# Performance work log

Measured on AMD Instinct MI355X. Metric: run time of the kernel, lower is better.

Reference implementation:

```python
import jax, jax.numpy as jnp
import numpy as np

B, S, D, H = 4, 2048, 1024, 16
DK = D // H
THETA = 10000.0


def apply_rope(x, pos, theta):
    # x: [B, H, S, DK], pos: [S] int
    d = x.shape[-1]
    inv_freq = theta ** (-jnp.arange(0, d, 2, dtype=jnp.float32) / d)  # [d/2]
    ang = pos.astype(jnp.float32)[:, None] * inv_freq[None, :]          # [S, d/2]
    cos, sin = jnp.cos(ang), jnp.sin(ang)
    x1 = x[..., 0::2]
    x2 = x[..., 1::2]
    r1 = x1 * cos - x2 * sin
    r2 = x1 * sin + x2 * cos
    return jnp.stack([r1, r2], axis=-1).reshape(x.shape)


def setup_inputs() -> dict:
    key = jax.random.key(0)
    ks = jax.random.split(key, 5)
    scale = 1.0 / np.sqrt(D)
    x = jax.random.normal(ks[0], (B, S, D), dtype=jnp.float32)
    Wq = jax.random.normal(ks[1], (D, D), dtype=jnp.float32) * scale
    Wk = jax.random.normal(ks[2], (D, D), dtype=jnp.float32) * scale
    Wv = jax.random.normal(ks[3], (D, D), dtype=jnp.float32) * scale
    Wo = jax.random.normal(ks[4], (D, D), dtype=jnp.float32) * scale
    token_positions = jnp.arange(S, dtype=jnp.int32)
    return {"x": x, "token_positions": token_positions,
            "Wq": Wq, "Wk": Wk, "Wv": Wv, "Wo": Wo}


def reference(x, token_positions, Wq, Wk, Wv, Wo):
    b, s, d = x.shape
    # Linear (no bias), weight stored [out, in]: y = x @ W.T
    q = (x @ Wq.T).reshape(b, s, H, DK).transpose(0, 2, 1, 3)  # [B,H,S,DK]
    k = (x @ Wk.T).reshape(b, s, H, DK).transpose(0, 2, 1, 3)
    v = (x @ Wv.T).reshape(b, s, H, DK).transpose(0, 2, 1, 3)
    q = apply_rope(q, token_positions, THETA)
    k = apply_rope(k, token_positions, THETA)
    scores = jnp.einsum('bhqd,bhkd->bhqk', q, k) / jnp.sqrt(jnp.float32(DK))
    causal = jnp.tril(jnp.ones((s, s), dtype=bool))
    scores = jnp.where(causal, scores, -jnp.inf)
    attn = jax.nn.softmax(scores, axis=-1)
    out = jnp.einsum('bhqk,bhkd->bhqd', attn, v)
    out = out.transpose(0, 2, 1, 3).reshape(b, s, d)
    return out @ Wo.T
```

## Files before the change

### kernel.cpp

```cpp
#include <hip/hip_runtime.h>

typedef unsigned short u16;
typedef __bf16 bf16x8 __attribute__((ext_vector_type(8)));
typedef float f32x4 __attribute__((ext_vector_type(4)));
typedef u16 u16x8 __attribute__((ext_vector_type(8)));
typedef u16 u16x4 __attribute__((ext_vector_type(4)));
typedef short s16x4 __attribute__((ext_vector_type(4)));

union V8 { u16x8 u; bf16x8 b; };
union V4 { u16x4 u; s16x4 s; unsigned w[2]; };

#define NB 4
#define NS 2048
#define ND 1024
#define NH 16
#define NDK 64
#define LP 80
#define CP 136
#define QSCL 0.18033688011112042f
#define FMAX 20.0f

__device__ __forceinline__ u16 f2bf(float f) {
  union { float f; unsigned u; } v; v.f = f;
  return (u16)((v.u + 0x7fffu + ((v.u >> 16) & 1u)) >> 16);
}

__device__ __forceinline__ unsigned pk2bf(float a, float b) {
#if __has_builtin(__builtin_amdgcn_cvt_pk_bf16_f32)
  auto v = __builtin_amdgcn_cvt_pk_bf16_f32(a, b);
  unsigned r; __builtin_memcpy(&r, &v, 4);
  return r;
#else
  return (unsigned)f2bf(a) | ((unsigned)f2bf(b) << 16);
#endif
}

__device__ __forceinline__ float fexp2(float x) {
#if __has_builtin(__builtin_amdgcn_exp2f)
  return __builtin_amdgcn_exp2f(x);
#else
  return exp2f(x);
#endif
}

__device__ __forceinline__ bf16x8 lds_frag(const u16* p) {
  V8 t; t.u = *(const u16x8*)p; return t.b;
}

__global__ __launch_bounds__(256) void cvt_bf16(const float* __restrict__ s,
                                                u16* __restrict__ d, int n) {
  const int i = (blockIdx.x * 256 + threadIdx.x) * 8;
  if (i >= n) return;
  const f32x4 lo = *(const f32x4*)(s + i);
  const f32x4 hi = *(const f32x4*)(s + i + 4);
  union { unsigned w[4]; u16x8 v; } o;
  o.w[0] = pk2bf(lo[0], lo[1]);
  o.w[1] = pk2bf(lo[2], lo[3]);
  o.w[2] = pk2bf(hi[0], hi[1]);
  o.w[3] = pk2bf(hi[2], hi[3]);
  *(u16x8*)(d + i) = o.v;
}

__global__ __launch_bounds__(256) void cvt_w4(const float* __restrict__ w0,
                                              const float* __restrict__ w1,
                                              const float* __restrict__ w2,
                                              const float* __restrict__ w3,
                                              u16* __restrict__ d) {
  const float* s = (blockIdx.y == 0) ? w0 : (blockIdx.y == 1) ? w1
                 : (blockIdx.y == 2) ? w2 : w3;
  const int i = (blockIdx.x * 256 + threadIdx.x) * 8;
  const f32x4 lo = *(const f32x4*)(s + i);
  const f32x4 hi = *(const f32x4*)(s + i + 4);
  union { unsigned w[4]; u16x8 v; } o;
  o.w[0] = pk2bf(lo[0], lo[1]);
  o.w[1] = pk2bf(lo[2], lo[3]);
  o.w[2] = pk2bf(hi[0], hi[1]);
  o.w[3] = pk2bf(hi[2], hi[3]);
  *(u16x8*)(d + (size_t)blockIdx.y * ND * ND + i) = o.v;
}

__global__ __launch_bounds__(256) void rope_tbl(const int* __restrict__ tp,
                                                float2* __restrict__ tbl) {
  const int i = blockIdx.x * 256 + threadIdx.x;
  const int s = i >> 5, d = i & 31;
  const float inv = __expf(-(float)d * 0.28782313662425572f);
  const float ang = (float)tp[s] * inv;
  float sn, cs;
  __sincosf(ang, &sn, &cs);
  tbl[i] = make_float2(cs, sn);
}

__global__ __launch_bounds__(256) void gemm_qkv(
    const u16* __restrict__ X, const u16* __restrict__ W0,
    const u16* __restrict__ W1, const u16* __restrict__ W2,
    void* __restrict__ O0, void* __restrict__ O1, void* __restrict__ O2,
    const float2* __restrict__ tbl, int modebase) {
  __shared__ u16 smem[2 * 128 * LP];
  u16* ldsA = smem;
  u16* ldsB = smem + 128 * LP;
  const int tid = threadIdx.x;
  const int lane = tid & 63;
  const int w = tid >> 6;
  const int quad = lane >> 4;
  const int l15 = lane & 15;
  const int z = blockIdx.z;
  const u16* Wp = (z == 0) ? W0 : (z == 1) ? W1 : W2;
  void* Op = (z == 0) ? O0 : (z == 1) ? O1 : O2;
  const int mode = modebase + z;
  const int m0 = blockIdx.x * 128;
  const int n0 = blockIdx.y * 128;
  const int wm = (w >> 1) * 64;
  const int wn = (w & 1) * 64;

  const int srow = tid >> 3;
  const int scol = (tid & 7) * 8;
  const u16* Ag = X + (size_t)(m0 + srow) * ND + scol;
  const u16* Bg = Wp + (size_t)(n0 + srow) * ND + scol;

  f32x4 acc[4][4];
  const f32x4 z4 = {0.f, 0.f, 0.f, 0.f};
  for (int i = 0; i < 4; i++)
    for (int j = 0; j < 4; j++) acc[i][j] = z4;

  for (int k0 = 0; k0 < ND; k0 += 64) {
    u16x8 ar[4], br[4];
    for (int r = 0; r < 4; r++) {
      ar[r] = *(const u16x8*)(Ag + (size_t)r * 32 * ND + k0);
      br[r] = *(const u16x8*)(Bg + (size_t)r * 32 * ND + k0);
    }
    __syncthreads();
    for (int r = 0; r < 4; r++) {
      *(u16x8*)&ldsA[(r * 32 + srow) * LP + scol] = ar[r];
      *(u16x8*)&ldsB[(r * 32 + srow) * LP + scol] = br[r];
    }
    __syncthreads();
    for (int kk = 0; kk < 2; kk++) {
      bf16x8 af[4], bfr[4];
      for (int mt = 0; mt < 4; mt++)
        af[mt] = lds_frag(&ldsA[(wm + mt * 16 + l15) * LP + (kk * 4 + quad) * 8]);
      for (int nt = 0; nt < 4; nt++)
        bfr[nt] = lds_frag(&ldsB[(wn + nt * 16 + l15) * LP + (kk * 4 + quad) * 8]);
      for (int mt = 0; mt < 4; mt++)
        for (int nt = 0; nt < 4; nt++)
          acc[mt][nt] = __builtin_amdgcn_mfma_f32_16x16x32_bf16(
              af[mt], bfr[nt], acc[mt][nt], 0, 0, 0);
    }
  }
  __syncthreads();

  if (mode < 2) {
    u16* cb = smem;
    for (int nt = 0; nt < 4; nt++) {
      const int n_g = n0 + wn + nt * 16 + l15;
      const int dk = n_g & 63;
      const float sgn = (dk & 1) ? 1.f : -1.f;
      const int d2 = dk >> 1;
      for (int mt = 0; mt < 4; mt++) {
        const int mrow = wm + mt * 16 + quad * 4;
        for (int r = 0; r < 4; r++) {
          const int m_g = m0 + mrow + r;
          float v = acc[mt][nt][r];
          const int s_i = m_g & (NS - 1);
          const float partner = __shfl_xor(v, 1);
          const float2 t = tbl[s_i * 32 + d2];
          v = v * t.x + partner * t.y * sgn;
          if (mode == 0) v *= QSCL;
          cb[(mrow + r) * CP + wn + nt * 16 + l15] = f2bf(v);
        }
      }
    }
    __syncthreads();
    const int c = (tid & 15) * 8;
    const int h = (n0 + c) >> 6;
    const int dk0 = (n0 + c) & 63;
    for (int p = 0; p < 8; p++) {
      const int row = p * 16 + (tid >> 4);
      const int m_g = m0 + row;
      const int b = m_g >> 11;
      const int s_i = m_g & (NS - 1);
      *(u16x8*)&((u16*)Op)[(size_t)(((b * NH) + h) * NS + s_i) * NDK + dk0] =
          *(const u16x8*)&cb[row * CP + c];
    }
  } else if (mode == 2) {
    u16* cbT = smem;
    for (int nt = 0; nt < 4; nt++)
      for (int mt = 0; mt < 4; mt++)
        for (int r = 0; r < 4; r++)
          cbT[(wn + nt * 16 + l15) * CP + wm + mt * 16 + quad * 4 + r] =
              f2bf(acc[mt][nt][r]);
    __syncthreads();
    const int b = m0 >> 11;
    const int s0 = m0 & (NS - 1);
    const int col = (tid & 15) * 8;
    for (int p = 0; p < 8; p++) {
      const int row = p * 16 + (tid >> 4);
      const int dkg = n0 + row;
      const int h = dkg >> 6;
      *(u16x8*)&((u16*)Op)[(size_t)(((b * NH) + h) * NDK + (dkg & 63)) * NS +
                           s0 + col] = *(const u16x8*)&cbT[row * CP + col];
    }
  } else {
    for (int nt = 0; nt < 4; nt++) {
      const int n_g = n0 + wn + nt * 16 + l15;
      for (int mt = 0; mt < 4; mt++) {
        const int mb = m0 + wm + mt * 16 + quad * 4;
        for (int r = 0; r < 4; r++)
          ((float*)Op)[(size_t)(mb + r) * ND + n_g] = acc[mt][nt][r];
      }
    }
  }
}

__global__ __launch_bounds__(512, 2) void attn(const u16* __restrict__ Q,
                                               const u16* __restrict__ Kc,
                                               const u16* __restrict__ Vt,
                                               u16* __restrict__ AO,
                                               unsigned* __restrict__ ctr) {
  __shared__ u16 smem[2 * 64 * LP];
  u16* kt = smem;
  u16* vt = smem + 64 * LP;
  __shared__ unsigned s_item;
  const int tid = threadIdx.x;
  const int lane = tid & 63;
  const int w = tid >> 6;
  const int quad = lane >> 4;
  const int l15 = lane & 15;

  int koff[2][4];
#pragma unroll
  for (int kk = 0; kk < 2; kk++)
#pragma unroll
    for (int nt = 0; nt < 4; nt++) {
      const int row = nt * 16 + l15;
      koff[kk][nt] = row * LP + (((kk * 4 + quad) ^ (row & 7)) * 8);
    }
  int voff[4][4];
#pragma unroll
  for (int dt = 0; dt < 4; dt++) {
    const int dk = dt * 16 + l15;
    const int xr = dk & 7;
#pragma unroll
    for (int nt = 0; nt < 4; nt++) {
      const int chunk = 2 * nt + (quad >> 1);
      voff[dt][nt] = dk * LP + ((chunk ^ xr) * 8) + 4 * (quad & 1);
    }
  }
  const int srow = tid >> 3;
  const int sg = tid & 7;
  const int woff = srow * LP + ((sg ^ (srow & 7)) * 8);

  for (int rep = 0; rep < 2; ++rep) {
    __syncthreads();
    if (tid == 0) s_item = atomicAdd(ctr, 1u) & 1023u;
    __syncthreads();
    const unsigned item = s_item;
    const int qt = 15 - (int)(item >> 6);
    const int bh = (int)(item & 63u);
    const int q0 = qt * 128;
    const int qg = q0 + w * 16 + l15;
    const int qmin = q0 + w * 16;

    const u16* Qb = Q + (size_t)bh * NS * NDK + (size_t)qg * NDK + quad * 8;
    const bf16x8 qf0 = lds_frag(Qb);
    const bf16x8 qf1 = lds_frag(Qb + 32);

    f32x4 oacc[4];
    const f32x4 z4 = {0.f, 0.f, 0.f, 0.f};
#pragma unroll
    for (int i = 0; i < 4; i++) oacc[i] = z4;
    float ls0 = 0.f, ls1 = 0.f;

    const u16* Kb = Kc + (size_t)bh * NS * NDK;
    const u16* Vg = Vt + (size_t)bh * NDK * NS;

    u16x8 kreg = *(const u16x8*)(Kb + (size_t)srow * NDK + sg * 8);
    u16x8 vreg = *(const u16x8*)(Vg + (size_t)srow * NS + sg * 8);

    const int jend = q0 + 64;
    const f32x4 nF = {-FMAX, -FMAX, -FMAX, -FMAX};
    for (int j0 = 0; j0 <= jend; j0 += 64) {
      __syncthreads();
      *(u16x8*)&kt[woff] = kreg;
      *(u16x8*)&vt[woff] = vreg;
      __syncthreads();
      if (j0 + 64 <= jend) {
        const int nj = j0 + 64;
        kreg = *(const u16x8*)(Kb + (size_t)(nj + srow) * NDK + sg * 8);
        vreg = *(const u16x8*)(Vg + (size_t)srow * NS + nj + sg * 8);
      }

      if (j0 <= qmin + 15) {
        f32x4 sa[4];
#pragma unroll
        for (int i = 0; i < 4; i++) sa[i] = nF;
        __builtin_amdgcn_s_setprio(1);
#pragma unroll
        for (int kk = 0; kk < 2; kk++) {
          const bf16x8 qf = kk ? qf1 : qf0;
#pragma unroll
          for (int nt = 0; nt < 4; nt++) {
            const bf16x8 kf = lds_frag(&kt[koff[kk][nt]]);
            sa[nt] = __builtin_amdgcn_mfma_f32_16x16x32_bf16(kf, qf, sa[nt], 0, 0, 0);
          }
        }
        __builtin_amdgcn_s_setprio(0);

        float p[4][4];
#pragma unroll
        for (int nt = 0; nt < 4; nt++)
#pragma unroll
          for (int r = 0; r < 4; r++) p[nt][r] = fexp2(sa[nt][r]);
        if (j0 + 63 > qmin) {
#pragma unroll
          for (int nt = 0; nt < 4; nt++)
#pragma unroll
            for (int r = 0; r < 4; r++)
              if ((j0 + nt * 16 + quad * 4 + r) > qg) p[nt][r] = 0.f;
        }
        {
          float s0 = (p[0][0] + p[0][1]) + (p[0][2] + p[0][3]);
          float s1 = (p[1][0] + p[1][1]) + (p[1][2] + p[1][3]);
          float s2 = (p[2][0] + p[2][1]) + (p[2][2] + p[2][3]);
          float s3 = (p[3][0] + p[3][1]) + (p[3][2] + p[3][3]);
          ls0 += s0 + s1;
          ls1 += s2 + s3;
        }

        s16x4 pa[4];
#pragma unroll
        for (int nt = 0; nt < 4; nt++) {
          V4 t;
          t.w[0] = pk2bf(p[nt][0], p[nt][1]);
          t.w[1] = pk2bf(p[nt][2], p[nt][3]);
          pa[nt] = t.s;
        }

        __builtin_amdgcn_s_setprio(1);
#pragma unroll
        for (int dt = 0; dt < 4; dt++) {
#pragma unroll
          for (int nt = 0; nt < 4; nt++) {
            V4 t;
            t.u = *(const u16x4*)&vt[voff[dt][nt]];
            oacc[dt] = __builtin_amdgcn_mfma_f32_16x16x16bf16_1k(pa[nt], t.s,
                                                                 oacc[dt], 0, 0, 0);
          }
        }
        __builtin_amdgcn_s_setprio(0);
      }
    }

    float lsum = ls0 + ls1;
    lsum += __shfl_xor(lsum, 16);
    lsum += __shfl_xor(lsum, 32);
    float lq[4];
#pragma unroll
    for (int r = 0; r < 4; r++) lq[r] = __shfl(lsum, quad * 4 + r);

    __syncthreads();
    u16* ob = smem;
#pragma unroll
    for (int dt = 0; dt < 4; dt++)
#pragma unroll
      for (int r = 0; r < 4; r++)
        ob[(w * 16 + quad * 4 + r) * 72 + dt * 16 + l15] =
            f2bf(oacc[dt][r] / lq[r]);
    __syncthreads();
    const int b = bh >> 4, h = bh & 15;
#pragma unroll
    for (int p2 = 0; p2 < 2; p2++) {
      const int idx = p2 * 512 + tid;
      const int row = idx >> 3;
      const int c = (idx & 7) * 8;
      *(u16x8*)&AO[(size_t)(b * NS + q0 + row) * ND + h * 64 + c] =
          *(const u16x8*)&ob[row * 72 + c];
    }
  }
}

extern "C" void kernel_launch(void* const* d_in, const int* in_sizes, int n_in,
                              void* d_out, int out_size, void* d_ws, size_t ws_size,
                              hipStream_t stream) {
  const float* x = (const float*)d_in[0];
  const int* tp = (const int*)d_in[1];
  const float* Wq = (const float*)d_in[2];
  const float* Wk = (const float*)d_in[3];
  const float* Wv = (const float*)d_in[4];
  const float* Wo = (const float*)d_in[5];

  const size_t NE = (size_t)NB * NS * ND;
  const int NW = ND * ND;
  u16* Qb = (u16*)d_ws;
  u16* Kb = Qb + NE;
  u16* Vtb = Kb + NE;
  u16* Xbf = Vtb + NE;
  u16* Wbf = Xbf + NE;
  u16* wend = Wbf + 4 * (size_t)NW;
  unsigned* ctr = (unsigned*)wend;
  float2* tbl = (float2*)(wend + 8);

  dim3 blk(256);
  cvt_bf16<<<dim3((unsigned)(NE / 2048)), blk, 0, stream>>>(x, Xbf, (int)NE);
  cvt_w4<<<dim3(NW / 2048, 4), blk, 0, stream>>>(Wq, Wk, Wv, Wo, Wbf);
  rope_tbl<<<dim3(256), blk, 0, stream>>>(tp, tbl);
  gemm_qkv<<<dim3(64, 8, 3), blk, 0, stream>>>(
      Xbf, Wbf, Wbf + (size_t)NW, Wbf + 2 * (size_t)NW, Qb, Kb, Vtb, tbl, 0);
  attn<<<dim3(512), dim3(512), 0, stream>>>(Qb, Kb, Vtb, Xbf, ctr);
  gemm_qkv<<<dim3(64, 8, 1), blk, 0, stream>>>(
      Xbf, Wbf + 3 * (size_t)NW, Wbf + 3 * (size_t)NW, Wbf + 3 * (size_t)NW,
      d_out, d_out, d_out, tbl, 3);
}
```

Measured before the change: 268.3 us.

## Launch one attention work item per block with higher occupancy target

The attention kernel now processes a single (q-tile, head) work item per block and launches 1024 blocks instead of 512 persistent blocks that each looped over two items. Launch bounds rise from 2 to 4 blocks per CU, and the precomputed LDS offset arrays are replaced by a few base offsets plus constant strides. The softmax exponentials, masking and bf16 packing are fused into one loop so fewer values stay live. Together these aim to cut register pressure so more waves fit per CU to hide latency. The trade-off is possible spilling or a worse instruction schedule under the tighter register budget, and the atomic work counter still sets the order in which tiles are processed.

Result: slower. 281.9 us (+5.1%).

```diff
diff --git a/kernel.cpp b/kernel.cpp
--- a/kernel.cpp
+++ b/kernel.cpp
@@ -211,7 +211,7 @@
   }
 }
 
-__global__ __launch_bounds__(512, 2) void attn(const u16* __restrict__ Q,
+__global__ __launch_bounds__(512, 4) void attn(const u16* __restrict__ Q,
                                                const u16* __restrict__ Kc,
                                                const u16* __restrict__ Vt,
                                                u16* __restrict__ AO,
@@ -226,155 +226,134 @@
   const int quad = lane >> 4;
   const int l15 = lane & 15;
 
-  int koff[2][4];
-#pragma unroll
-  for (int kk = 0; kk < 2; kk++)
-#pragma unroll
-    for (int nt = 0; nt < 4; nt++) {
-      const int row = nt * 16 + l15;
-      koff[kk][nt] = row * LP + (((kk * 4 + quad) ^ (row & 7)) * 8);
-    }
-  int voff[4][4];
-#pragma unroll
-  for (int dt = 0; dt < 4; dt++) {
-    const int dk = dt * 16 + l15;
-    const int xr = dk & 7;
-#pragma unroll
-    for (int nt = 0; nt < 4; nt++) {
-      const int chunk = 2 * nt + (quad >> 1);
-      voff[dt][nt] = dk * LP + ((chunk ^ xr) * 8) + 4 * (quad & 1);
-    }
-  }
+  if (tid == 0) s_item = atomicAdd(ctr, 1u) & 1023u;
+  __syncthreads();
+  const unsigned item = s_item;
+  const int qt = 15 - (int)(item >> 6);
+  const int bh = (int)(item & 63u);
+  const int q0 = qt * 128;
+  const int qg = q0 + w * 16 + l15;
+  const int qmin = q0 + w * 16;
+
+  const int x7 = l15 & 7;
+  const int kb0 = l15 * LP + ((quad ^ x7) * 8);
+  const int kb1 = l15 * LP + (((4 + quad) ^ x7) * 8);
+  int vb[4];
+#pragma unroll
+  for (int nt = 0; nt < 4; nt++)
+    vb[nt] = l15 * LP + (((2 * nt + (quad >> 1)) ^ x7) * 8) + 4 * (quad & 1);
   const int srow = tid >> 3;
   const int sg = tid & 7;
   const int woff = srow * LP + ((sg ^ (srow & 7)) * 8);
 
-  for (int rep = 0; rep < 2; ++rep) {
-    __syncthreads();
-    if (tid == 0) s_item = atomicAdd(ctr, 1u) & 1023u;
-    __syncthreads();
-    const unsigned item = s_item;
-    const int qt = 15 - (int)(item >> 6);
-    const int bh = (int)(item & 63u);
-    const int q0 = qt * 128;
-    const int qg = q0 + w * 16 + l15;
-    const int qmin = q0 + w * 16;
-
-    const u16* Qb = Q + (size_t)bh * NS * NDK + (size_t)qg * NDK + quad * 8;
-    const bf16x8 qf0 = lds_frag(Qb);
-    const bf16x8 qf1 = lds_frag(Qb + 32);
-
-    f32x4 oacc[4];
-    const f32x4 z4 = {0.f, 0.f, 0.f, 0.f};
-#pragma unroll
-    for (int i = 0; i < 4; i++) oacc[i] = z4;
-    float ls0 = 0.f, ls1 = 0.f;
-
-    const u16* Kb = Kc + (size_t)bh * NS * NDK;
-    const u16* Vg = Vt + (size_t)bh * NDK * NS;
-
-    u16x8 kreg = *(const u16x8*)(Kb + (size_t)srow * NDK + sg * 8);
-    u16x8 vreg = *(const u16x8*)(Vg + (size_t)srow * NS + sg * 8);
-
-    const int jend = q0 + 64;
-    const f32x4 nF = {-FMAX, -FMAX, -FMAX, -FMAX};
-    for (int j0 = 0; j0 <= jend; j0 += 64) {
-      __syncthreads();
-      *(u16x8*)&kt[woff] = kreg;
-      *(u16x8*)&vt[woff] = vreg;
-      __syncthreads();
-      if (j0 + 64 <= jend) {
-        const int nj = j0 + 64;
-        kreg = *(const u16x8*)(Kb + (size_t)(nj + srow) * NDK + sg * 8);
-        vreg = *(const u16x8*)(Vg + (size_t)srow * NS + nj + sg * 8);
-      }
-
-      if (j0 <= qmin + 15) {
-        f32x4 sa[4];
-#pragma unroll
-        for (int i = 0; i < 4; i++) sa[i] = nF;
-        __builtin_amdgcn_s_setprio(1);
-#pragma unroll
-        for (int kk = 0; kk < 2; kk++) {
-          const bf16x8 qf = kk ? qf1 : qf0;
-#pragma unroll
-          for (int nt = 0; nt < 4; nt++) {
-            const bf16x8 kf = lds_frag(&kt[koff[kk][nt]]);
-            sa[nt] = __builtin_amdgcn_mfma_f32_16x16x32_bf16(kf, qf, sa[nt], 0, 0, 0);
-          }
+  const u16* Qb = Q + (size_t)bh * NS * NDK + (size_t)qg * NDK + quad * 8;
+  const bf16x8 qf0 = lds_frag(Qb);
+  const bf16x8 qf1 = lds_frag(Qb + 32);
+
+  f32x4 oacc[4];
+  const f32x4 z4 = {0.f, 0.f, 0.f, 0.f};
+#pragma unroll
+  for (int i = 0; i < 4; i++) oacc[i] = z4;
+  float ls0 = 0.f, ls1 = 0.f;
+
+  const u16* Kb = Kc + (size_t)bh * NS * NDK;
+  const u16* Vg = Vt + (size_t)bh * NDK * NS;
+
+  u16x8 kreg = *(const u16x8*)(Kb + (size_t)srow * NDK + sg * 8);
+  u16x8 vreg = *(const u16x8*)(Vg + (size_t)srow * NS + sg * 8);
+
+  const int jend = q0 + 64;
+  const f32x4 nF = {-FMAX, -FMAX, -FMAX, -FMAX};
+  for (int j0 = 0; j0 <= jend; j0 += 64) {
+    __syncthreads();
+    *(u16x8*)&kt[woff] = kreg;
+    *(u16x8*)&vt[woff] = vreg;
+    __syncthreads();
+    if (j0 + 64 <= jend) {
+      const int nj = j0 + 64;
+      kreg = *(const u16x8*)(Kb + (size_t)(nj + srow) * NDK + sg * 8);
+      vreg = *(const u16x8*)(Vg + (size_t)srow * NS + nj + sg * 8);
+    }
+
+    if (j0 <= qmin + 15) {
+      f32x4 sa[4];
+#pragma unroll
+      for (int i = 0; i < 4; i++) sa[i] = nF;
+      __builtin_amdgcn_s_setprio(1);
+#pragma unroll
+      for (int nt = 0; nt < 4; nt++) {
+        const bf16x8 kf0 = lds_frag(&kt[kb0 + nt * (16 * LP)]);
+        sa[nt] = __builtin_amdgcn_mfma_f32_16x16x32_bf16(kf0, qf0, sa[nt], 0, 0, 0);
+      }
+#pragma unroll
+      for (int nt = 0; nt < 4; nt++) {
+        const bf16x8 kf1 = lds_frag(&kt[kb1 + nt * (16 * LP)]);
+        sa[nt] = __builtin_amdgcn_mfma_f32_16x16x32_bf16(kf1, qf1, sa[nt], 0, 0, 0);
+      }
+      __builtin_amdgcn_s_setprio(0);
+
+      const bool domask = (j0 + 63 > qmin);
+      s16x4 pa[4];
+#pragma unroll
+      for (int nt = 0; nt < 4; nt++) {
+        float p0 = fexp2(sa[nt][0]);
+        float p1 = fexp2(sa[nt][1]);
+        float p2 = fexp2(sa[nt][2]);
+        float p3 = fexp2(sa[nt][3]);
+        if (domask) {
+          const int kbase = j0 + nt * 16 + quad * 4;
+          if (kbase + 0 > qg) p0 = 0.f;
+          if (kbase + 1 > qg) p1 = 0.f;
+          if (kbase + 2 > qg) p2 = 0.f;
+          if (kbase + 3 > qg) p3 = 0.f;
         }
-        __builtin_amdgcn_s_setprio(0);
-
-        float p[4][4];
-#pragma unroll
-        for (int nt = 0; nt < 4; nt++)
-#pragma unroll
-          for (int r = 0; r < 4; r++) p[nt][r] = fexp2(sa[nt][r]);
-        if (j0 + 63 > qmin) {
-#pragma unroll
-          for (int nt = 0; nt < 4; nt++)
-#pragma unroll
-            for (int r = 0; r < 4; r++)
-              if ((j0 + nt * 16 + quad * 4 + r) > qg) p[nt][r] = 0.f;
-        }
-        {
-          float s0 = (p[0][0] + p[0][1]) + (p[0][2] + p[0][3]);
-          float s1 = (p[1][0] + p[1][1]) + (p[1][2] + p[1][3]);
-          float s2 = (p[2][0] + p[2][1]) + (p[2][2] + p[2][3]);
-          float s3 = (p[3][0] + p[3][1]) + (p[3][2] + p[3][3]);
-          ls0 += s0 + s1;
-          ls1 += s2 + s3;
-        }
-
-        s16x4 pa[4];
+        ls0 += p0 + p1;
+        ls1 += p2 + p3;
+        V4 t;
+        t.w[0] = pk2bf(p0, p1);
+        t.w[1] = pk2bf(p2, p3);
+        pa[nt] = t.s;
+      }
+
+      __builtin_amdgcn_s_setprio(1);
+#pragma unroll
+      for (int dt = 0; dt < 4; dt++) {
 #pragma unroll
         for (int nt = 0; nt < 4; nt++) {
           V4 t;
-          t.w[0] = pk2bf(p[nt][0], p[nt][1]);
-          t.w[1] = pk2bf(p[nt][2], p[nt][3]);
-          pa[nt] = t.s;
+          t.u = *(const u16x4*)&vt[vb[nt] + dt * (16 * LP)];
+          oacc[dt] = __builtin_amdgcn_mfma_f32_16x16x16bf16_1k(pa[nt], t.s,
+                                                               oacc[dt], 0, 0, 0);
         }
-
-        __builtin_amdgcn_s_setprio(1);
-#pragma unroll
-        for (int dt = 0; dt < 4; dt++) {
-#pragma unroll
-          for (int nt = 0; nt < 4; nt++) {
-            V4 t;
-            t.u = *(const u16x4*)&vt[voff[dt][nt]];
-            oacc[dt] = __builtin_amdgcn_mfma_f32_16x16x16bf16_1k(pa[nt], t.s,
-                                                                 oacc[dt], 0, 0, 0);
-          }
-        }
-        __builtin_amdgcn_s_setprio(0);
-      }
-    }
-
-    float lsum = ls0 + ls1;
-    lsum += __shfl_xor(lsum, 16);
-    lsum += __shfl_xor(lsum, 32);
-    float lq[4];
-#pragma unroll
-    for (int r = 0; r < 4; r++) lq[r] = __shfl(lsum, quad * 4 + r);
-
-    __syncthreads();
-    u16* ob = smem;
-#pragma unroll
-    for (int dt = 0; dt < 4; dt++)
-#pragma unroll
-      for (int r = 0; r < 4; r++)
-        ob[(w * 16 + quad * 4 + r) * 72 + dt * 16 + l15] =
-            f2bf(oacc[dt][r] / lq[r]);
-    __syncthreads();
-    const int b = bh >> 4, h = bh & 15;
-#pragma unroll
-    for (int p2 = 0; p2 < 2; p2++) {
-      const int idx = p2 * 512 + tid;
-      const int row = idx >> 3;
-      const int c = (idx & 7) * 8;
-      *(u16x8*)&AO[(size_t)(b * NS + q0 + row) * ND + h * 64 + c] =
-          *(const u16x8*)&ob[row * 72 + c];
-    }
+      }
+      __builtin_amdgcn_s_setprio(0);
+    }
+  }
+
+  float lsum = ls0 + ls1;
+  lsum += __shfl_xor(lsum, 16);
+  lsum += __shfl_xor(lsum, 32);
+  float lq[4];
+#pragma unroll
+  for (int r = 0; r < 4; r++) lq[r] = __shfl(lsum, quad * 4 + r);
+
+  __syncthreads();
+  u16* ob = smem;
+#pragma unroll
+  for (int dt = 0; dt < 4; dt++)
+#pragma unroll
+    for (int r = 0; r < 4; r++)
+      ob[(w * 16 + quad * 4 + r) * 72 + dt * 16 + l15] =
+          f2bf(oacc[dt][r] / lq[r]);
+  __syncthreads();
+  const int b = bh >> 4, h = bh & 15;
+#pragma unroll
+  for (int p2 = 0; p2 < 2; p2++) {
+    const int idx = p2 * 512 + tid;
+    const int row = idx >> 3;
+    const int c = (idx & 7) * 8;
+    *(u16x8*)&AO[(size_t)(b * NS + q0 + row) * ND + h * 64 + c] =
+        *(const u16x8*)&ob[row * 72 + c];
   }
 }
 
@@ -405,7 +384,7 @@
   rope_tbl<<<dim3(256), blk, 0, stream>>>(tp, tbl);
   gemm_qkv<<<dim3(64, 8, 3), blk, 0, stream>>>(
       Xbf, Wbf, Wbf + (size_t)NW, Wbf + 2 * (size_t)NW, Qb, Kb, Vtb, tbl, 0);
-  attn<<<dim3(512), dim3(512), 0, stream>>>(Qb, Kb, Vtb, Xbf, ctr);
+  attn<<<dim3(1024), dim3(512), 0, stream>>>(Qb, Kb, Vtb, Xbf, ctr);
   gemm_qkv<<<dim3(64, 8, 1), blk, 0, stream>>>(
       Xbf, Wbf + 3 * (size_t)NW, Wbf + 3 * (size_t)NW, Wbf + 3 * (size_t)NW,
       d_out, d_out, d_out, tbl, 3);
```
